# Performance work log

Measured on AMD Instinct MI355X. Metric: run time of the kernel, lower is better.

Reference implementation:

```python
import jax, jax.numpy as jnp
import numpy as np
import math

M = 512          # num_bin_x
NB = 512         # num_bin_y
NUM_NODES = 2_000_000
K = 4            # max bins a node can overlap per dim (size <= 2.5 bins)
SQRT2 = math.sqrt(2.0)


def setup_inputs() -> dict:
    key = jax.random.key(0)
    k1, k2 = jax.random.split(key)
    node_pos = jax.random.uniform(k1, (NUM_NODES, 2), jnp.float32, 0.05, 0.95)
    # node sizes between 0.5 and 2.5 bins (normalized layout units)
    node_size = jax.random.uniform(k2, (NUM_NODES, 2), jnp.float32) * (2.0 / M) + (0.5 / M)
    return {
        "node_pos": node_pos,
        "node_size": node_size,
        "node_weight": jnp.ones((NUM_NODES,), jnp.float32),
        "expand_ratio": jnp.ones((NUM_NODES,), jnp.float32),
        "unit_len": jnp.array([1.0 / M, 1.0 / NB], jnp.float32),
        "init_density_map": jnp.zeros((M, NB), jnp.float32),
        "num_bin_x": M,
        "num_bin_y": NB,
    }


def pre_normalize(node_pos, node_size, node_weight, expand_ratio, unit_len, mx, ny):
    # density_map_cuda.pre_normalize: expand tiny nodes to sqrt(2)*unit_len,
    # rescale weight to preserve area, convert rects to bin coordinates.
    ux, uy = unit_len[0], unit_len[1]
    w, h = node_size[:, 0], node_size[:, 1]
    new_w = jnp.maximum(w, SQRT2 * ux)
    new_h = jnp.maximum(h, SQRT2 * uy)
    weight = node_weight * expand_ratio * (w * h) / (new_w * new_h)
    xl = jnp.clip((node_pos[:, 0] - 0.5 * new_w) / ux, 0.0, mx)
    xh = jnp.clip((node_pos[:, 0] + 0.5 * new_w) / ux, 0.0, mx)
    yl = jnp.clip((node_pos[:, 1] - 0.5 * new_h) / uy, 0.0, ny)
    yh = jnp.clip((node_pos[:, 1] + 0.5 * new_h) / uy, 0.0, ny)
    return jnp.stack([xl, xh, yl, yh, weight], axis=1)  # [N, 5]


def scatter_density(info, mx, ny):
    # density_map_cuda.forward: overlap-area scatter-add of node rects into bins.
    xl, xh, yl, yh, w = info[:, 0], info[:, 1], info[:, 2], info[:, 3], info[:, 4]
    bx0 = jnp.floor(xl).astype(jnp.int32)
    by0 = jnp.floor(yl).astype(jnp.int32)
    dm = jnp.zeros((mx, ny), jnp.float32)
    for dx in range(K):
        ix = bx0 + dx
        fx = ix.astype(jnp.float32)
        ox = jnp.clip(jnp.minimum(xh, fx + 1.0) - jnp.maximum(xl, fx), 0.0)
        ixc = jnp.clip(ix, 0, mx - 1)
        for dy in range(K):
            iy = by0 + dy
            fy = iy.astype(jnp.float32)
            oy = jnp.clip(jnp.minimum(yh, fy + 1.0) - jnp.maximum(yl, fy), 0.0)
            iyc = jnp.clip(iy, 0, ny - 1)
            dm = dm.at[ixc, iyc].add(w * ox * oy)
    return dm


def make_transforms(n):
    k = jnp.arange(n, dtype=jnp.float32)[:, None]
    m = jnp.arange(n, dtype=jnp.float32)[None, :]
    ang = jnp.pi * k * (2.0 * m + 1.0) / (2.0 * n)
    C = jnp.cos(ang)  # [freq, space]
    S = jnp.sin(ang)
    w = jnp.where(jnp.arange(n) == 0, 1.0, 2.0).astype(jnp.float32)
    return C, S, w


def spectral_solve(dm, unit_len, mx, ny):
    # fft_scale construction from __init__
    wj = (jnp.arange(mx, dtype=jnp.float32) * (2.0 * jnp.pi / mx))[:, None]
    wk = (jnp.arange(ny, dtype=jnp.float32) * (2.0 * jnp.pi / ny))[None, :]
    wk = wk * (unit_len[0] / unit_len[1])  # scale_w_k=True
    wsq = wj ** 2 + wk ** 2
    wsq = wsq.at[0, 0].set(1.0)
    pscale = (1.0 / wsq).at[0, 0].set(0.0)
    fx_scale = wj * pscale * 0.5
    fy_scale = wk * pscale * 0.5

    Cx, Sx, wx = make_transforms(mx)
    Cy, Sy, wy = make_transforms(ny)
    # dct2: coeff[u,v] = (1/(M*N)) * sum_{m,n} dm[m,n] cos(pi u(2m+1)/2M) cos(pi v(2n+1)/2N)
    coeff = (Cx @ dm @ Cy.T) / (mx * ny)
    ICx = (wx[:, None] * Cx)  # weighted inverse cosine basis [freq, space]
    ICy = (wy[:, None] * Cy)
    ISx = (wx[:, None] * Sx)
    ISy = (wy[:, None] * Sy)
    potential = ICx.T @ (coeff * pscale) @ ICy          # idct2
    force_x = ISx.T @ (coeff * fx_scale) @ ICy          # idxst_idct
    force_y = ICx.T @ (coeff * fy_scale) @ ISy          # idct_idxst
    return potential, force_x, force_y


def reference(node_pos, node_size, node_weight, expand_ratio, unit_len,
              init_density_map, num_bin_x, num_bin_y):
    info = pre_normalize(node_pos, node_size, node_weight, expand_ratio,
                         unit_len, num_bin_x, num_bin_y)
    density_map = init_density_map + scatter_density(info, num_bin_x, num_bin_y)
    potential, _, _ = spectral_solve(density_map, unit_len, num_bin_x, num_bin_y)
    energy = jnp.sum(potential * density_map)
    return energy
```

## Files before the change

### kernel.cpp

```cpp
#include <hip/hip_runtime.h>
#include <math.h>

#define MX 512
#define NY 512
#define TWO_PI 6.283185307179586f

#define TSHIFT 6
#define NT 64
#define LDIM 68
#define SLAB (LDIM * LDIM)
#define SLAB4 (SLAB / 4)
#define NPB 2048
#define KPT 8
#define CAP 40960
#define TTARGET 1216
#define RPARTS 19
#define QSCALE 26214.0f
#define QINV (1.0f / 26214.0f)

typedef __attribute__((ext_vector_type(8))) short short8;
typedef __attribute__((ext_vector_type(4))) float float4_t;
typedef __attribute__((ext_vector_type(4))) unsigned short ushort4_t;

__device__ __forceinline__ unsigned short f2bf(float x) {
    union { float f; unsigned u; } v; v.f = x;
    unsigned r = v.u + 0x7fffu + ((v.u >> 16) & 1u);
    return (unsigned short)(r >> 16);
}
__device__ __forceinline__ float bf2f(unsigned short h) {
    union { float f; unsigned u; } v; v.u = ((unsigned)h) << 16;
    return v.f;
}

__device__ __forceinline__ void node_bounds(float2 p, float2 s, float ux, float uy,
                                            float& xl, float& xh, float& yl, float& yh,
                                            float& nw, float& nh) {
    const float SQ2 = 1.41421356237309515f;
    nw = fmaxf(s.x, SQ2 * ux);
    nh = fmaxf(s.y, SQ2 * uy);
    xl = fminf(fmaxf((p.x - 0.5f * nw) / ux, 0.0f), (float)MX);
    xh = fminf(fmaxf((p.x + 0.5f * nw) / ux, 0.0f), (float)MX);
    yl = fminf(fmaxf((p.y - 0.5f * nh) / uy, 0.0f), (float)NY);
    yh = fminf(fmaxf((p.y + 0.5f * nh) / uy, 0.0f), (float)NY);
}

__global__ void gen_cos_kernel(unsigned short* __restrict__ Ch,
                               unsigned short* __restrict__ Cl,
                               unsigned int* __restrict__ base,
                               unsigned int* __restrict__ cursor,
                               float* __restrict__ out, int cap_mode) {
    int idx = blockIdx.x * blockDim.x + threadIdx.x;
    if (idx == 0) *out = 0.0f;
    if (cap_mode && idx <= NT) {
        base[idx] = (unsigned int)idx * CAP;
        if (idx < NT) cursor[idx] = (unsigned int)idx * CAP;
    }
    int a = idx >> 9;
    int j = idx & 511;
    float x = cospif((float)(a * (2 * j + 1)) * (1.0f / 1024.0f));
    unsigned short hi = f2bf(x);
    Ch[idx] = hi;
    Cl[idx] = f2bf(x - bf2f(hi));
}

__global__ __launch_bounds__(256)
void count_kernel(const float2* __restrict__ pos, const float2* __restrict__ size,
                  const float* __restrict__ unit_len,
                  unsigned int* __restrict__ cnt, int n) {
    __shared__ unsigned int h[NT];
    if (threadIdx.x < NT) h[threadIdx.x] = 0;
    __syncthreads();
    float ux = unit_len[0], uy = unit_len[1];
    int start = blockIdx.x * NPB;
    int end = min(start + NPB, n);
#pragma unroll
    for (int k = 0; k < KPT; k++) {
        int i = start + k * 256 + (int)threadIdx.x;
        if (i < end) {
            float xl, xh, yl, yh, nw, nh;
            node_bounds(pos[i], size[i], ux, uy, xl, xh, yl, yh, nw, nh);
            int bx0 = min((int)floorf(xl), MX - 1);
            int by0 = min((int)floorf(yl), NY - 1);
            atomicAdd(&h[((bx0 >> TSHIFT) << 3) | (by0 >> TSHIFT)], 1u);
        }
    }
    __syncthreads();
    if (threadIdx.x < NT) {
        unsigned int c = h[threadIdx.x];
        if (c) atomicAdd(&cnt[threadIdx.x], c);
    }
}

__global__ void scan_kernel(const unsigned int* __restrict__ cnt,
                            unsigned int* __restrict__ base,
                            unsigned int* __restrict__ cursor) {
    if (threadIdx.x == 0 && blockIdx.x == 0) {
        unsigned int ex = 0;
        for (int t = 0; t < NT; t++) {
            base[t] = ex;
            cursor[t] = ex;
            ex += cnt[t];
        }
        base[NT] = ex;
    }
}

__global__ __launch_bounds__(256)
void place_kernel(const float2* __restrict__ pos, const float2* __restrict__ size,
                  const float* __restrict__ nwt, const float* __restrict__ er,
                  const float* __restrict__ unit_len,
                  const unsigned int* __restrict__ base,
                  unsigned int* __restrict__ cursor,
                  float4* __restrict__ pb, int n) {
    __shared__ unsigned int h[NT];
    __shared__ unsigned int lb[NT + 1];
    __shared__ unsigned int bb[NT];
    __shared__ float4 buf[NPB];
    __shared__ unsigned char til[NPB];
    if (threadIdx.x < NT) h[threadIdx.x] = 0;
    __syncthreads();
    float ux = unit_len[0], uy = unit_len[1];
    int start = blockIdx.x * NPB;
    int end = min(start + NPB, n);

    float cxl[KPT], cyl[KPT], cw[KPT];
    unsigned int cq[KPT], pk[KPT];
#pragma unroll
    for (int k = 0; k < KPT; k++) {
        int i = start + k * 256 + (int)threadIdx.x;
        if (i < end) {
            float2 p = pos[i], s = size[i];
            float xl, xh, yl, yh, nw, nh;
            node_bounds(p, s, ux, uy, xl, xh, yl, yh, nw, nh);
            cxl[k] = xl; cyl[k] = yl;
            cw[k] = nwt[i] * er[i] * (s.x * s.y) / (nw * nh);
            unsigned qx = (unsigned)((xh - xl) * QSCALE + 0.5f);
            unsigned qy = (unsigned)((yh - yl) * QSCALE + 0.5f);
            if (qx > 65535u) qx = 65535u;
            if (qy > 65535u) qy = 65535u;
            cq[k] = qx | (qy << 16);
            int bx0 = min((int)floorf(xl), MX - 1);
            int by0 = min((int)floorf(yl), NY - 1);
            unsigned int t = ((bx0 >> TSHIFT) << 3) | (by0 >> TSHIFT);
            pk[k] = (t << 11) | atomicAdd(&h[t], 1u);
        }
    }
    __syncthreads();
    if (threadIdx.x < NT) {
        unsigned int c = h[threadIdx.x];
        unsigned int S = c;
#pragma unroll
        for (int d = 1; d < 64; d <<= 1) {
            unsigned int v = __shfl_up(S, d, 64);
            if ((int)threadIdx.x >= d) S += v;
        }
        lb[threadIdx.x] = S - c;
        if (threadIdx.x == NT - 1) lb[NT] = S;
        bb[threadIdx.x] = c ? atomicAdd(&cursor[threadIdx.x], c) : 0u;
    }
    __syncthreads();
#pragma unroll
    for (int k = 0; k < KPT; k++) {
        int i = start + k * 256 + (int)threadIdx.x;
        if (i < end) {
            unsigned int t = pk[k] >> 11;
            unsigned int slot = lb[t] + (pk[k] & 2047u);
            buf[slot] = make_float4(cxl[k], cyl[k], cw[k], __uint_as_float(cq[k]));
            til[slot] = (unsigned char)t;
        }
    }
    __syncthreads();
    unsigned int total = lb[NT];
    for (unsigned int j = threadIdx.x; j < total; j += 256) {
        unsigned int t = til[j];
        unsigned int dst = bb[t] + (j - lb[t]);
        if (dst < base[t + 1]) pb[dst] = buf[j];
    }
}

__device__ __forceinline__ void accum_one(float4 v, float* acc, int tbx, int tby) {
    float xl = v.x, yl = v.y, w = v.z;
    unsigned q = __float_as_uint(v.w);
    float xh = xl + (float)(q & 0xffffu) * QINV;
    float yh = yl + (float)(q >> 16) * QINV;
    int bx0 = min((int)floorf(xl), MX - 1);
    int by0 = min((int)floorf(yl), NY - 1);
    float oxs[4], oys[4];
    int rb[4], lys[4];
#pragma unroll
    for (int d = 0; d < 4; d++) {
        int ix = bx0 + d;
        float fx = (float)ix;
        oxs[d] = fmaxf(fminf(xh, fx + 1.0f) - fmaxf(xl, fx), 0.0f);
        rb[d] = (min(ix, MX - 1) - tbx) * LDIM;
        int iy = by0 + d;
        float fy = (float)iy;
        oys[d] = fmaxf(fminf(yh, fy + 1.0f) - fmaxf(yl, fy), 0.0f);
        lys[d] = min(iy, NY - 1) - tby;
    }
#pragma unroll
    for (int dx = 0; dx < 4; dx++) {
        if (oxs[dx] == 0.0f) continue;
        float wox = w * oxs[dx];
#pragma unroll
        for (int dy = 0; dy < 4; dy++) {
            float vv = wox * oys[dy];
            if (vv != 0.0f) atomicAdd(&acc[rb[dx] + lys[dy]], vv);
        }
    }
}

__global__ __launch_bounds__(256)
void accum_kernel(const float4* __restrict__ pb,
                  const unsigned int* __restrict__ base,
                  const unsigned int* __restrict__ cursor,
                  float* __restrict__ slab, int T) {
    __shared__ float acc[SLAB];
    __shared__ int sh_t, sh_done;
    __shared__ unsigned int sh_ks, sh_ke, sh_b0;
    int tid = threadIdx.x;
    if (tid < 64) {
        unsigned int t = tid;
        unsigned int b0 = base[t];
        unsigned int cap = base[t + 1] - b0;
        unsigned int cr = cursor[t] - b0;
        unsigned int c = cr < cap ? cr : cap;
        unsigned int S = c;
#pragma unroll
        for (int d = 1; d < 64; d <<= 1) {
            unsigned int v = __shfl_up(S, d, 64);
            if (tid >= d) S += v;
        }
        unsigned int total = __shfl(S, 63, 64);
        unsigned int nb = total ? (unsigned int)(((unsigned long long)c * (unsigned int)T) / total) + 1u : 1u;
        unsigned int Pn = nb;
#pragma unroll
        for (int d = 1; d < 64; d <<= 1) {
            unsigned int v = __shfl_up(Pn, d, 64);
            if (tid >= d) Pn += v;
        }
        unsigned int NBU = __shfl(Pn, 63, 64);
        unsigned int Pex = Pn - nb;
        unsigned int b = blockIdx.x;
        if (tid == 0) sh_done = (b >= NBU) ? 1 : 0;
        if (b >= Pex && b < Pn) {
            unsigned int s = b - Pex;
            unsigned int chunk = nb ? (c + nb - 1) / nb : 0u;
            unsigned int ks = s * chunk;
            unsigned int ke = min(c, ks + chunk);
            sh_t = (int)t; sh_ks = ks; sh_ke = ke; sh_b0 = b0;
        }
    }
    for (int e = tid; e < SLAB4; e += 256)
        ((float4*)acc)[e] = make_float4(0.f, 0.f, 0.f, 0.f);
    __syncthreads();
    if (sh_done) return;

    int t = sh_t;
    int tbx = (t >> 3) << TSHIFT;
    int tby = (t & 7) << TSHIFT;
    unsigned int b0 = sh_b0;
    unsigned int ke = sh_ke;

    unsigned int k = sh_ks + (unsigned int)tid;
    float4 cur = make_float4(0.f, 0.f, 0.f, 0.f);
    bool have = (k < ke);
    if (have) cur = pb[b0 + k];
    while (have) {
        unsigned int k2 = k + 256;
        bool have2 = (k2 < ke);
        float4 nxt = make_float4(0.f, 0.f, 0.f, 0.f);
        if (have2) nxt = pb[b0 + k2];
        accum_one(cur, acc, tbx, tby);
        cur = nxt; k = k2; have = have2;
    }
    __syncthreads();

    float4* dst = (float4*)(slab + (size_t)blockIdx.x * SLAB);
    for (int e = tid; e < SLAB4; e += 256)
        dst[e] = ((float4*)acc)[e];
}

__global__ __launch_bounds__(256)
void reduce_slabs_kernel(const float* __restrict__ slab,
                         float* __restrict__ tacc,
                         const unsigned int* __restrict__ base,
                         const unsigned int* __restrict__ cursor, int T) {
    __shared__ unsigned int sh_P, sh_nb;
    int t = blockIdx.x / RPARTS;
    int part = blockIdx.x - t * RPARTS;
    int tid = threadIdx.x;
    if (tid < 64) {
        unsigned int tt = tid;
        unsigned int b0 = base[tt];
        unsigned int cap = base[tt + 1] - b0;
        unsigned int cr = cursor[tt] - b0;
        unsigned int c = cr < cap ? cr : cap;
        unsigned int S = c;
#pragma unroll
        for (int d = 1; d < 64; d <<= 1) {
            unsigned int v = __shfl_up(S, d, 64);
            if (tid >= d) S += v;
        }
        unsigned int total = __shfl(S, 63, 64);
        unsigned int nb = total ? (unsigned int)(((unsigned long long)c * (unsigned int)T) / total) + 1u : 1u;
        unsigned int Pn = nb;
#pragma unroll
        for (int d = 1; d < 64; d <<= 1) {
            unsigned int v = __shfl_up(Pn, d, 64);
            if (tid >= d) Pn += v;
        }
        if ((int)tt == t) { sh_P = Pn - nb; sh_nb = nb; }
    }
    __syncthreads();
    int e = part * 256 + tid;
    if (e < SLAB) {
        const float* s0 = slab + (size_t)sh_P * SLAB + e;
        float sum = 0.0f;
        unsigned int nb = sh_nb;
        for (unsigned int s = 0; s < nb; s++) sum += s0[(size_t)s * SLAB];
        tacc[(size_t)t * SLAB + e] = sum;
    }
}

__global__ __launch_bounds__(256)
void combine_kernel(const float* __restrict__ tacc,
                    const float* __restrict__ init_dm,
                    unsigned short* __restrict__ dmh,
                    unsigned short* __restrict__ dml) {
    int v = blockIdx.x * blockDim.x + threadIdx.x;
    int gx = v >> 7;
    int g4 = v & 127;
    int gy = g4 << 2;
    int rx = gx & 63, ry = gy & 63;
    int tx0 = gx >> TSHIFT, ty0 = gy >> TSHIFT;

    float4 sum = ((const float4*)init_dm)[v];
#pragma unroll
    for (int ax = 0; ax < 2; ax++) {
        int tx = tx0 - ax;
        if (tx < 0 || (ax == 1 && rx > 3)) continue;
        int lx = rx + (ax << TSHIFT);
#pragma unroll
        for (int ay = 0; ay < 2; ay++) {
            int ty = ty0 - ay;
            if (ty < 0 || (ay == 1 && ry > 0)) continue;
            int ly = ry + (ay << TSHIFT);
            float4 sv = *(const float4*)(tacc
                + (size_t)((tx << 3) | ty) * SLAB + lx * LDIM + ly);
            sum.x += sv.x; sum.y += sv.y; sum.z += sv.z; sum.w += sv.w;
        }
    }
    ushort4_t hi, lo;
    float sv[4] = {sum.x, sum.y, sum.z, sum.w};
#pragma unroll
    for (int r = 0; r < 4; r++) {
        unsigned short h = f2bf(sv[r]);
        hi[r] = h;
        lo[r] = f2bf(sv[r] - bf2f(h));
    }
    int idx = (gx << 9) | gy;
    *(ushort4_t*)(dmh + idx) = hi;
    *(ushort4_t*)(dml + idx) = lo;
}

__global__ __launch_bounds__(256)
void scatter_kernel(const float2* __restrict__ pos, const float2* __restrict__ size,
                    const float* __restrict__ nwt, const float* __restrict__ er,
                    const float* __restrict__ unit_len,
                    float* __restrict__ dm, int n) {
    int i = blockIdx.x * blockDim.x + threadIdx.x;
    if (i >= n) return;
    float ux = unit_len[0], uy = unit_len[1];
    float2 p = pos[i], s = size[i];
    float xl, xh, yl, yh, nw, nh;
    node_bounds(p, s, ux, uy, xl, xh, yl, yh, nw, nh);
    float w = nwt[i] * er[i] * (s.x * s.y) / (nw * nh);
    int bx0 = (int)floorf(xl);
    int by0 = (int)floorf(yl);
#pragma unroll
    for (int dx = 0; dx < 4; dx++) {
        int ix = bx0 + dx;
        float fx = (float)ix;
        float ox = fmaxf(fminf(xh, fx + 1.0f) - fmaxf(xl, fx), 0.0f);
        if (ox == 0.0f) continue;
        int rowoff = min(max(ix, 0), MX - 1) * NY;
        float wox = w * ox;
#pragma unroll
        for (int dy = 0; dy < 4; dy++) {
            int iy = by0 + dy;
            float fy = (float)iy;
            float oy = fmaxf(fminf(yh, fy + 1.0f) - fmaxf(yl, fy), 0.0f);
            float vv = wox * oy;
            if (vv != 0.0f) atomicAdd(&dm[rowoff + min(max(iy, 0), NY - 1)], vv);
        }
    }
}

__global__ void cvt_dm_kernel(const float* __restrict__ dm,
                              unsigned short* __restrict__ dmh,
                              unsigned short* __restrict__ dml) {
    int idx = blockIdx.x * blockDim.x + threadIdx.x;
    float x = dm[idx];
    unsigned short hi = f2bf(x);
    dmh[idx] = hi;
    dml[idx] = f2bf(x - bf2f(hi));
}

__global__ __launch_bounds__(256)
void dct1_mfma_kernel(const unsigned short* __restrict__ dmh,
                      const unsigned short* __restrict__ dml,
                      const unsigned short* __restrict__ Ch,
                      const unsigned short* __restrict__ Cl,
                      unsigned short* __restrict__ UhT,
                      unsigned short* __restrict__ UlT) {
    int lane = threadIdx.x & 63;
    int wv = threadIdx.x >> 6;
    int tile = blockIdx.x * 4 + wv;
    int jt = (tile >> 5) * 16;
    int bt = (tile & 31) * 16;
    int m = lane & 15, q = lane >> 4;
    float4_t acc = {0.f, 0.f, 0.f, 0.f};
    const unsigned short* ah_row = dmh + (jt + m) * 512;
    const unsigned short* al_row = dml + (jt + m) * 512;
    const unsigned short* bh_row = Ch + (bt + m) * 512;
    const unsigned short* bl_row = Cl + (bt + m) * 512;
#pragma unroll 4
    for (int k0 = 0; k0 < 512; k0 += 32) {
        int off = k0 + q * 8;
        short8 ah = *(const short8*)(ah_row + off);
        short8 al = *(const short8*)(al_row + off);
        short8 bh = *(const short8*)(bh_row + off);
        short8 bl = *(const short8*)(bl_row + off);
        acc = __builtin_amdgcn_mfma_f32_16x16x32_bf16(ah, bh, acc, 0, 0, 0);
        acc = __builtin_amdgcn_mfma_f32_16x16x32_bf16(ah, bl, acc, 0, 0, 0);
        acc = __builtin_amdgcn_mfma_f32_16x16x32_bf16(al, bh, acc, 0, 0, 0);
    }
#pragma unroll
    for (int r = 0; r < 4; r++) {
        float v = acc[r];
        unsigned short hi = f2bf(v);
        int addr = (bt + m) * 512 + jt + q * 4 + r;
        UhT[addr] = hi;
        UlT[addr] = f2bf(v - bf2f(hi));
    }
}

__global__ __launch_bounds__(256)
void dct2_mfma_kernel(const unsigned short* __restrict__ Ch,
                      const unsigned short* __restrict__ Cl,
                      const unsigned short* __restrict__ UhT,
                      const unsigned short* __restrict__ UlT,
                      const float* __restrict__ unit_len,
                      float* __restrict__ out) {
    __shared__ float red[4];
    int lane = threadIdx.x & 63;
    int wv = threadIdx.x >> 6;
    int tile = blockIdx.x * 4 + wv;
    int at = (tile >> 5) * 16;
    int bt = (tile & 31) * 16;
    int m = lane & 15, q = lane >> 4;
    float4_t acc = {0.f, 0.f, 0.f, 0.f};
    const unsigned short* ah_row = Ch + (at + m) * 512;
    const unsigned short* al_row = Cl + (at + m) * 512;
    const unsigned short* bh_row = UhT + (bt + m) * 512;
    const unsigned short* bl_row = UlT + (bt + m) * 512;
#pragma unroll 4
    for (int k0 = 0; k0 < 512; k0 += 32) {
        int off = k0 + q * 8;
        short8 ah = *(const short8*)(ah_row + off);
        short8 al = *(const short8*)(al_row + off);
        short8 bh = *(const short8*)(bh_row + off);
        short8 bl = *(const short8*)(bl_row + off);
        acc = __builtin_amdgcn_mfma_f32_16x16x32_bf16(ah, bh, acc, 0, 0, 0);
        acc = __builtin_amdgcn_mfma_f32_16x16x32_bf16(ah, bl, acc, 0, 0, 0);
        acc = __builtin_amdgcn_mfma_f32_16x16x32_bf16(al, bh, acc, 0, 0, 0);
    }
    float ratio = unit_len[0] / unit_len[1];
    int b = bt + m;
    float wkb = (float)b * (TWO_PI / (float)NY) * ratio;
    float wyb = (b == 0) ? 1.0f : 2.0f;
    float e = 0.0f;
#pragma unroll
    for (int r = 0; r < 4; r++) {
        int a = at + q * 4 + r;
        float wja = (float)a * (TWO_PI / (float)MX);
        float wsq = wja * wja + wkb * wkb;
        float ps = (a == 0 && b == 0) ? 0.0f : (1.0f / wsq);
        float wxa = (a == 0) ? 1.0f : 2.0f;
        e += wxa * wyb * ps * acc[r] * acc[r];
    }
#pragma unroll
    for (int off = 32; off > 0; off >>= 1) e += __shfl_down(e, off, 64);
    if (lane == 0) red[wv] = e;
    __syncthreads();
    if (threadIdx.x == 0) {
        float t = red[0] + red[1] + red[2] + red[3];
        atomicAdd(out, t * (1.0f / ((float)MX * (float)NY)));
    }
}

extern "C" void kernel_launch(void* const* d_in, const int* in_sizes, int n_in,
                              void* d_out, int out_size, void* d_ws, size_t ws_size,
                              hipStream_t stream) {
    const float2* node_pos  = (const float2*)d_in[0];
    const float2* node_size = (const float2*)d_in[1];
    const float*  node_wt   = (const float*)d_in[2];
    const float*  exp_ratio = (const float*)d_in[3];
    const float*  unit_len  = (const float*)d_in[4];
    const float*  init_dm   = (const float*)d_in[5];
    float* out = (float*)d_out;
    int n = in_sizes[2];

    char* wsb = (char*)d_ws;
    size_t off = 0;
    auto alloc = [&](size_t bytes) { void* p = wsb + off; off = (off + bytes + 255) & ~(size_t)255; return p; };
    unsigned short* Ch   = (unsigned short*)alloc((size_t)MX * NY * 2);
    unsigned short* Cl   = (unsigned short*)alloc((size_t)MX * NY * 2);
    unsigned short* dmh  = (unsigned short*)alloc((size_t)MX * NY * 2);
    unsigned short* dml  = (unsigned short*)alloc((size_t)MX * NY * 2);
    unsigned short* UhT  = (unsigned short*)alloc((size_t)MX * NY * 2);
    unsigned short* UlT  = (unsigned short*)alloc((size_t)MX * NY * 2);
    float*          dm     = (float*)alloc((size_t)MX * NY * sizeof(float));
    unsigned int*   cnt    = (unsigned int*)alloc(NT * sizeof(unsigned int));
    unsigned int*   tbase  = (unsigned int*)alloc((NT + 1) * sizeof(unsigned int));
    unsigned int*   cursor = (unsigned int*)alloc(NT * sizeof(unsigned int));
    float*          tacc   = (float*)alloc((size_t)NT * SLAB * sizeof(float));
    size_t off_common = off;
    size_t slab_bytes = (size_t)SLAB * sizeof(float);

    float4* pbF = (float4*)alloc((size_t)NT * CAP * sizeof(float4));
    int TF = 0;
    float* slbF = nullptr;
    if (off <= ws_size) {
        size_t navail = (ws_size - off) / slab_bytes;
        if (navail >= 320) {
            size_t t = navail - 64;
            TF = (int)(t > TTARGET ? TTARGET : t);
            slbF = (float*)alloc((size_t)(TF + 64) * slab_bytes);
        }
    }
    bool tierFast = (slbF != nullptr);

    off = off_common;
    float4* pbE = (float4*)alloc((size_t)n * sizeof(float4));
    int TE = 0;
    float* slbE = nullptr;
    if (off <= ws_size) {
        size_t navail = (ws_size - off) / slab_bytes;
        if (navail >= 128) {
            size_t t = navail - 64;
            TE = (int)(t > TTARGET ? TTARGET : t);
            slbE = (float*)alloc((size_t)(TE + 64) * slab_bytes);
        }
    }
    bool tierExact = (slbE != nullptr);

    gen_cos_kernel<<<(MX * NY) / 256, 256, 0, stream>>>(Ch, Cl, tbase, cursor,
                                                        out, tierFast ? 1 : 0);

    if (tierFast || tierExact) {
        float4* pb  = tierFast ? pbF : pbE;
        float*  slb = tierFast ? slbF : slbE;
        int     T   = tierFast ? TF : TE;
        int nblk = (n + NPB - 1) / NPB;
        if (!tierFast) {
            hipMemsetAsync(cnt, 0, NT * sizeof(unsigned int), stream);
            count_kernel<<<nblk, 256, 0, stream>>>(node_pos, node_size, unit_len, cnt, n);
            scan_kernel<<<1, 64, 0, stream>>>(cnt, tbase, cursor);
        }
        place_kernel<<<nblk, 256, 0, stream>>>(
            node_pos, node_size, node_wt, exp_ratio, unit_len, tbase, cursor, pb, n);
        accum_kernel<<<T + 64, 256, 0, stream>>>(pb, tbase, cursor, slb, T);
        reduce_slabs_kernel<<<NT * RPARTS, 256, 0, stream>>>(slb, tacc, tbase, cursor, T);
        combine_kernel<<<256, 256, 0, stream>>>(tacc, init_dm, dmh, dml);
    } else {
        hipMemcpyAsync(dm, init_dm, (size_t)MX * NY * sizeof(float),
                       hipMemcpyDeviceToDevice, stream);
        scatter_kernel<<<(n + 255) / 256, 256, 0, stream>>>(
            node_pos, node_size, node_wt, exp_ratio, unit_len, dm, n);
        cvt_dm_kernel<<<(MX * NY) / 256, 256, 0, stream>>>(dm, dmh, dml);
    }

    dct1_mfma_kernel<<<256, 256, 0, stream>>>(dmh, dml, Ch, Cl, UhT, UlT);
    dct2_mfma_kernel<<<256, 256, 0, stream>>>(Ch, Cl, UhT, UlT, unit_len, out);
}
```

Measured before the change: 235.0 us.

## Fuse reduce, combine, cosine gen and both DCT stages into one cooperative kernel

On the fast tier, the cosine-table generation, slab reduction, tile combine, and the two MFMA DCT passes are merged into one cooperative kernel that uses grid.sync between phases. Per-tile buffers are now addressed at fixed offsets of t*CAP, with cursors zeroed by a memset, so the separate init of base/cursor goes away. This cuts several kernel launches and their inter-kernel gaps. The cost is that the whole pipeline runs on only 256 blocks with grid-wide barriers, and the slab reduction now runs serially per element.

New measurement: 356.9 us. +51.8%, slower.

```diff
diff --git a/kernel.cpp b/kernel.cpp
--- a/kernel.cpp
+++ b/kernel.cpp
@@ -1,5 +1,8 @@
 #include <hip/hip_runtime.h>
+#include <hip/hip_cooperative_groups.h>
 #include <math.h>
+
+namespace cg = cooperative_groups;
 
 #define MX 512
 #define NY 512
@@ -17,6 +20,7 @@
 #define RPARTS 19
 #define QSCALE 26214.0f
 #define QINV (1.0f / 26214.0f)
+#define NBLK_MEGA 256
 
 typedef __attribute__((ext_vector_type(8))) short short8;
 typedef __attribute__((ext_vector_type(4))) float float4_t;
@@ -44,79 +48,18 @@
     yh = fminf(fmaxf((p.y + 0.5f * nh) / uy, 0.0f), (float)NY);
 }
 
-__global__ void gen_cos_kernel(unsigned short* __restrict__ Ch,
-                               unsigned short* __restrict__ Cl,
-                               unsigned int* __restrict__ base,
-                               unsigned int* __restrict__ cursor,
-                               float* __restrict__ out, int cap_mode) {
-    int idx = blockIdx.x * blockDim.x + threadIdx.x;
-    if (idx == 0) *out = 0.0f;
-    if (cap_mode && idx <= NT) {
-        base[idx] = (unsigned int)idx * CAP;
-        if (idx < NT) cursor[idx] = (unsigned int)idx * CAP;
-    }
-    int a = idx >> 9;
-    int j = idx & 511;
-    float x = cospif((float)(a * (2 * j + 1)) * (1.0f / 1024.0f));
-    unsigned short hi = f2bf(x);
-    Ch[idx] = hi;
-    Cl[idx] = f2bf(x - bf2f(hi));
-}
-
 __global__ __launch_bounds__(256)
-void count_kernel(const float2* __restrict__ pos, const float2* __restrict__ size,
-                  const float* __restrict__ unit_len,
-                  unsigned int* __restrict__ cnt, int n) {
-    __shared__ unsigned int h[NT];
-    if (threadIdx.x < NT) h[threadIdx.x] = 0;
-    __syncthreads();
-    float ux = unit_len[0], uy = unit_len[1];
-    int start = blockIdx.x * NPB;
-    int end = min(start + NPB, n);
-#pragma unroll
-    for (int k = 0; k < KPT; k++) {
-        int i = start + k * 256 + (int)threadIdx.x;
-        if (i < end) {
-            float xl, xh, yl, yh, nw, nh;
-            node_bounds(pos[i], size[i], ux, uy, xl, xh, yl, yh, nw, nh);
-            int bx0 = min((int)floorf(xl), MX - 1);
-            int by0 = min((int)floorf(yl), NY - 1);
-            atomicAdd(&h[((bx0 >> TSHIFT) << 3) | (by0 >> TSHIFT)], 1u);
-        }
-    }
-    __syncthreads();
-    if (threadIdx.x < NT) {
-        unsigned int c = h[threadIdx.x];
-        if (c) atomicAdd(&cnt[threadIdx.x], c);
-    }
-}
-
-__global__ void scan_kernel(const unsigned int* __restrict__ cnt,
-                            unsigned int* __restrict__ base,
-                            unsigned int* __restrict__ cursor) {
-    if (threadIdx.x == 0 && blockIdx.x == 0) {
-        unsigned int ex = 0;
-        for (int t = 0; t < NT; t++) {
-            base[t] = ex;
-            cursor[t] = ex;
-            ex += cnt[t];
-        }
-        base[NT] = ex;
-    }
-}
-
-__global__ __launch_bounds__(256)
-void place_kernel(const float2* __restrict__ pos, const float2* __restrict__ size,
-                  const float* __restrict__ nwt, const float* __restrict__ er,
-                  const float* __restrict__ unit_len,
-                  const unsigned int* __restrict__ base,
-                  unsigned int* __restrict__ cursor,
-                  float4* __restrict__ pb, int n) {
+void place_fast_kernel(const float2* __restrict__ pos, const float2* __restrict__ size,
+                       const float* __restrict__ nwt, const float* __restrict__ er,
+                       const float* __restrict__ unit_len,
+                       unsigned int* __restrict__ cursor,
+                       float4* __restrict__ pb, float* __restrict__ out, int n) {
     __shared__ unsigned int h[NT];
     __shared__ unsigned int lb[NT + 1];
     __shared__ unsigned int bb[NT];
     __shared__ float4 buf[NPB];
     __shared__ unsigned char til[NPB];
+    if (blockIdx.x == 0 && threadIdx.x == 0) *out = 0.0f;
     if (threadIdx.x < NT) h[threadIdx.x] = 0;
     __syncthreads();
     float ux = unit_len[0], uy = unit_len[1];
@@ -174,7 +117,7 @@
     for (unsigned int j = threadIdx.x; j < total; j += 256) {
         unsigned int t = til[j];
         unsigned int dst = bb[t] + (j - lb[t]);
-        if (dst < base[t + 1]) pb[dst] = buf[j];
+        if (dst < CAP) pb[(size_t)t * CAP + dst] = buf[j];
     }
 }
 
@@ -207,6 +150,385 @@
             float vv = wox * oys[dy];
             if (vv != 0.0f) atomicAdd(&acc[rb[dx] + lys[dy]], vv);
         }
+    }
+}
+
+__global__ __launch_bounds__(256)
+void accum_fast_kernel(const float4* __restrict__ pb,
+                       const unsigned int* __restrict__ cursor,
+                       float* __restrict__ slab, int T) {
+    __shared__ float acc[SLAB];
+    __shared__ int sh_t, sh_done;
+    __shared__ unsigned int sh_ks, sh_ke;
+    int tid = threadIdx.x;
+    if (tid < 64) {
+        unsigned int t = tid;
+        unsigned int cr = cursor[t];
+        unsigned int c = cr < CAP ? cr : CAP;
+        unsigned int S = c;
+#pragma unroll
+        for (int d = 1; d < 64; d <<= 1) {
+            unsigned int v = __shfl_up(S, d, 64);
+            if (tid >= d) S += v;
+        }
+        unsigned int total = __shfl(S, 63, 64);
+        unsigned int nb = total ? (unsigned int)(((unsigned long long)c * (unsigned int)T) / total) + 1u : 1u;
+        unsigned int Pn = nb;
+#pragma unroll
+        for (int d = 1; d < 64; d <<= 1) {
+            unsigned int v = __shfl_up(Pn, d, 64);
+            if (tid >= d) Pn += v;
+        }
+        unsigned int NBU = __shfl(Pn, 63, 64);
+        unsigned int Pex = Pn - nb;
+        unsigned int b = blockIdx.x;
+        if (tid == 0) sh_done = (b >= NBU) ? 1 : 0;
+        if (b >= Pex && b < Pn) {
+            unsigned int s = b - Pex;
+            unsigned int chunk = nb ? (c + nb - 1) / nb : 0u;
+            unsigned int ks = s * chunk;
+            unsigned int ke = min(c, ks + chunk);
+            sh_t = (int)t; sh_ks = ks; sh_ke = ke;
+        }
+    }
+    for (int e = tid; e < SLAB4; e += 256)
+        ((float4*)acc)[e] = make_float4(0.f, 0.f, 0.f, 0.f);
+    __syncthreads();
+    if (sh_done) return;
+
+    int t = sh_t;
+    int tbx = (t >> 3) << TSHIFT;
+    int tby = (t & 7) << TSHIFT;
+    unsigned int b0 = (unsigned int)t * CAP;
+    unsigned int ke = sh_ke;
+
+    unsigned int k = sh_ks + (unsigned int)tid;
+    float4 cur = make_float4(0.f, 0.f, 0.f, 0.f);
+    bool have = (k < ke);
+    if (have) cur = pb[b0 + k];
+    while (have) {
+        unsigned int k2 = k + 256;
+        bool have2 = (k2 < ke);
+        float4 nxt = make_float4(0.f, 0.f, 0.f, 0.f);
+        if (have2) nxt = pb[b0 + k2];
+        accum_one(cur, acc, tbx, tby);
+        cur = nxt; k = k2; have = have2;
+    }
+    __syncthreads();
+
+    float4* dst = (float4*)(slab + (size_t)blockIdx.x * SLAB);
+    for (int e = tid; e < SLAB4; e += 256)
+        dst[e] = ((float4*)acc)[e];
+}
+
+__global__ __launch_bounds__(256, 1)
+void mega_kernel(const float* __restrict__ slab,
+                 const unsigned int* __restrict__ cursor, int T,
+                 const float* __restrict__ init_dm,
+                 unsigned short* __restrict__ Ch, unsigned short* __restrict__ Cl,
+                 unsigned short* __restrict__ dmh, unsigned short* __restrict__ dml,
+                 unsigned short* __restrict__ UhT, unsigned short* __restrict__ UlT,
+                 float* __restrict__ tacc,
+                 const float* __restrict__ unit_len, float* __restrict__ out) {
+    cg::grid_group grid = cg::this_grid();
+    __shared__ unsigned int shP[NT];
+    __shared__ unsigned int shNb[NT];
+    __shared__ float red[4];
+    int tid = threadIdx.x;
+    int bid = blockIdx.x;
+    int gid = bid * 256 + tid;
+
+    if (tid < 64) {
+        unsigned int tt = tid;
+        unsigned int cr = cursor[tt];
+        unsigned int c = cr < CAP ? cr : CAP;
+        unsigned int S = c;
+#pragma unroll
+        for (int d = 1; d < 64; d <<= 1) {
+            unsigned int v = __shfl_up(S, d, 64);
+            if (tid >= d) S += v;
+        }
+        unsigned int total = __shfl(S, 63, 64);
+        unsigned int nb = total ? (unsigned int)(((unsigned long long)c * (unsigned int)T) / total) + 1u : 1u;
+        unsigned int Pn = nb;
+#pragma unroll
+        for (int d = 1; d < 64; d <<= 1) {
+            unsigned int v = __shfl_up(Pn, d, 64);
+            if (tid >= d) Pn += v;
+        }
+        shP[tt] = Pn - nb;
+        shNb[tt] = nb;
+    }
+    __syncthreads();
+
+    for (int idx = gid; idx < MX * NY; idx += 65536) {
+        int a = idx >> 9;
+        int j = idx & 511;
+        float x = cospif((float)(a * (2 * j + 1)) * (1.0f / 1024.0f));
+        unsigned short hi = f2bf(x);
+        Ch[idx] = hi;
+        Cl[idx] = f2bf(x - bf2f(hi));
+    }
+    for (int x = gid; x < NT * SLAB; x += 65536) {
+        int t = x / SLAB;
+        int e = x - t * SLAB;
+        const float* s0 = slab + (size_t)shP[t] * SLAB + e;
+        float sum = 0.0f;
+        unsigned int nb = shNb[t];
+        for (unsigned int s = 0; s < nb; s++) sum += s0[(size_t)s * SLAB];
+        tacc[x] = sum;
+    }
+    grid.sync();
+
+    {
+        int v = gid;
+        int gx = v >> 7;
+        int g4 = v & 127;
+        int gy = g4 << 2;
+        int rx = gx & 63, ry = gy & 63;
+        int tx0 = gx >> TSHIFT, ty0 = gy >> TSHIFT;
+        float4 sum = ((const float4*)init_dm)[v];
+#pragma unroll
+        for (int ax = 0; ax < 2; ax++) {
+            int tx = tx0 - ax;
+            if (tx < 0 || (ax == 1 && rx > 3)) continue;
+            int lx = rx + (ax << TSHIFT);
+#pragma unroll
+            for (int ay = 0; ay < 2; ay++) {
+                int ty = ty0 - ay;
+                if (ty < 0 || (ay == 1 && ry > 0)) continue;
+                int ly = ry + (ay << TSHIFT);
+                float4 sv = *(const float4*)(tacc
+                    + (size_t)((tx << 3) | ty) * SLAB + lx * LDIM + ly);
+                sum.x += sv.x; sum.y += sv.y; sum.z += sv.z; sum.w += sv.w;
+            }
+        }
+        ushort4_t hi, lo;
+        float sv[4] = {sum.x, sum.y, sum.z, sum.w};
+#pragma unroll
+        for (int r = 0; r < 4; r++) {
+            unsigned short h = f2bf(sv[r]);
+            hi[r] = h;
+            lo[r] = f2bf(sv[r] - bf2f(h));
+        }
+        int idx = (gx << 9) | gy;
+        *(ushort4_t*)(dmh + idx) = hi;
+        *(ushort4_t*)(dml + idx) = lo;
+    }
+    grid.sync();
+
+    {
+        int lane = tid & 63;
+        int wv = tid >> 6;
+        int tile = bid * 4 + wv;
+        int jt = (tile >> 5) * 16;
+        int bt = (tile & 31) * 16;
+        int m = lane & 15, q = lane >> 4;
+        float4_t acc = {0.f, 0.f, 0.f, 0.f};
+        const unsigned short* ah_row = dmh + (jt + m) * 512;
+        const unsigned short* al_row = dml + (jt + m) * 512;
+        const unsigned short* bh_row = Ch + (bt + m) * 512;
+        const unsigned short* bl_row = Cl + (bt + m) * 512;
+#pragma unroll 4
+        for (int k0 = 0; k0 < 512; k0 += 32) {
+            int off = k0 + q * 8;
+            short8 ah = *(const short8*)(ah_row + off);
+            short8 al = *(const short8*)(al_row + off);
+            short8 bh = *(const short8*)(bh_row + off);
+            short8 bl = *(const short8*)(bl_row + off);
+            acc = __builtin_amdgcn_mfma_f32_16x16x32_bf16(ah, bh, acc, 0, 0, 0);
+            acc = __builtin_amdgcn_mfma_f32_16x16x32_bf16(ah, bl, acc, 0, 0, 0);
+            acc = __builtin_amdgcn_mfma_f32_16x16x32_bf16(al, bh, acc, 0, 0, 0);
+        }
+#pragma unroll
+        for (int r = 0; r < 4; r++) {
+            float v = acc[r];
+            unsigned short hi = f2bf(v);
+            int addr = (bt + m) * 512 + jt + q * 4 + r;
+            UhT[addr] = hi;
+            UlT[addr] = f2bf(v - bf2f(hi));
+        }
+    }
+    grid.sync();
+
+    {
+        int lane = tid & 63;
+        int wv = tid >> 6;
+        int tile = bid * 4 + wv;
+        int at = (tile >> 5) * 16;
+        int bt = (tile & 31) * 16;
+        int m = lane & 15, q = lane >> 4;
+        float4_t acc = {0.f, 0.f, 0.f, 0.f};
+        const unsigned short* ah_row = Ch + (at + m) * 512;
+        const unsigned short* al_row = Cl + (at + m) * 512;
+        const unsigned short* bh_row = UhT + (bt + m) * 512;
+        const unsigned short* bl_row = UlT + (bt + m) * 512;
+#pragma unroll 4
+        for (int k0 = 0; k0 < 512; k0 += 32) {
+            int off = k0 + q * 8;
+            short8 ah = *(const short8*)(ah_row + off);
+            short8 al = *(const short8*)(al_row + off);
+            short8 bh = *(const short8*)(bh_row + off);
+            short8 bl = *(const short8*)(bl_row + off);
+            acc = __builtin_amdgcn_mfma_f32_16x16x32_bf16(ah, bh, acc, 0, 0, 0);
+            acc = __builtin_amdgcn_mfma_f32_16x16x32_bf16(ah, bl, acc, 0, 0, 0);
+            acc = __builtin_amdgcn_mfma_f32_16x16x32_bf16(al, bh, acc, 0, 0, 0);
+        }
+        float ratio = unit_len[0] / unit_len[1];
+        int b = bt + m;
+        float wkb = (float)b * (TWO_PI / (float)NY) * ratio;
+        float wyb = (b == 0) ? 1.0f : 2.0f;
+        float e = 0.0f;
+#pragma unroll
+        for (int r = 0; r < 4; r++) {
+            int a = at + q * 4 + r;
+            float wja = (float)a * (TWO_PI / (float)MX);
+            float wsq = wja * wja + wkb * wkb;
+            float ps = (a == 0 && b == 0) ? 0.0f : (1.0f / wsq);
+            float wxa = (a == 0) ? 1.0f : 2.0f;
+            e += wxa * wyb * ps * acc[r] * acc[r];
+        }
+#pragma unroll
+        for (int off = 32; off > 0; off >>= 1) e += __shfl_down(e, off, 64);
+        if (lane == 0) red[wv] = e;
+        __syncthreads();
+        if (tid == 0) {
+            float t = red[0] + red[1] + red[2] + red[3];
+            atomicAdd(out, t * (1.0f / ((float)MX * (float)NY)));
+        }
+    }
+}
+
+__global__ void gen_cos_kernel(unsigned short* __restrict__ Ch,
+                               unsigned short* __restrict__ Cl,
+                               unsigned int* __restrict__ base,
+                               unsigned int* __restrict__ cursor,
+                               float* __restrict__ out, int cap_mode) {
+    int idx = blockIdx.x * blockDim.x + threadIdx.x;
+    if (idx == 0) *out = 0.0f;
+    if (cap_mode && idx <= NT) {
+        base[idx] = (unsigned int)idx * CAP;
+        if (idx < NT) cursor[idx] = (unsigned int)idx * CAP;
+    }
+    int a = idx >> 9;
+    int j = idx & 511;
+    float x = cospif((float)(a * (2 * j + 1)) * (1.0f / 1024.0f));
+    unsigned short hi = f2bf(x);
+    Ch[idx] = hi;
+    Cl[idx] = f2bf(x - bf2f(hi));
+}
+
+__global__ __launch_bounds__(256)
+void count_kernel(const float2* __restrict__ pos, const float2* __restrict__ size,
+                  const float* __restrict__ unit_len,
+                  unsigned int* __restrict__ cnt, int n) {
+    __shared__ unsigned int h[NT];
+    if (threadIdx.x < NT) h[threadIdx.x] = 0;
+    __syncthreads();
+    float ux = unit_len[0], uy = unit_len[1];
+    int start = blockIdx.x * NPB;
+    int end = min(start + NPB, n);
+#pragma unroll
+    for (int k = 0; k < KPT; k++) {
+        int i = start + k * 256 + (int)threadIdx.x;
+        if (i < end) {
+            float xl, xh, yl, yh, nw, nh;
+            node_bounds(pos[i], size[i], ux, uy, xl, xh, yl, yh, nw, nh);
+            int bx0 = min((int)floorf(xl), MX - 1);
+            int by0 = min((int)floorf(yl), NY - 1);
+            atomicAdd(&h[((bx0 >> TSHIFT) << 3) | (by0 >> TSHIFT)], 1u);
+        }
+    }
+    __syncthreads();
+    if (threadIdx.x < NT) {
+        unsigned int c = h[threadIdx.x];
+        if (c) atomicAdd(&cnt[threadIdx.x], c);
+    }
+}
+
+__global__ void scan_kernel(const unsigned int* __restrict__ cnt,
+                            unsigned int* __restrict__ base,
+                            unsigned int* __restrict__ cursor) {
+    if (threadIdx.x == 0 && blockIdx.x == 0) {
+        unsigned int ex = 0;
+        for (int t = 0; t < NT; t++) {
+            base[t] = ex;
+            cursor[t] = ex;
+            ex += cnt[t];
+        }
+        base[NT] = ex;
+    }
+}
+
+__global__ __launch_bounds__(256)
+void place_kernel(const float2* __restrict__ pos, const float2* __restrict__ size,
+                  const float* __restrict__ nwt, const float* __restrict__ er,
+                  const float* __restrict__ unit_len,
+                  const unsigned int* __restrict__ base,
+                  unsigned int* __restrict__ cursor,
+                  float4* __restrict__ pb, int n) {
+    __shared__ unsigned int h[NT];
+    __shared__ unsigned int lb[NT + 1];
+    __shared__ unsigned int bb[NT];
+    __shared__ float4 buf[NPB];
+    __shared__ unsigned char til[NPB];
+    if (threadIdx.x < NT) h[threadIdx.x] = 0;
+    __syncthreads();
+    float ux = unit_len[0], uy = unit_len[1];
+    int start = blockIdx.x * NPB;
+    int end = min(start + NPB, n);
+    float cxl[KPT], cyl[KPT], cw[KPT];
+    unsigned int cq[KPT], pk[KPT];
+#pragma unroll
+    for (int k = 0; k < KPT; k++) {
+        int i = start + k * 256 + (int)threadIdx.x;
+        if (i < end) {
+            float2 p = pos[i], s = size[i];
+            float xl, xh, yl, yh, nw, nh;
+            node_bounds(p, s, ux, uy, xl, xh, yl, yh, nw, nh);
+            cxl[k] = xl; cyl[k] = yl;
+            cw[k] = nwt[i] * er[i] * (s.x * s.y) / (nw * nh);
+            unsigned qx = (unsigned)((xh - xl) * QSCALE + 0.5f);
+            unsigned qy = (unsigned)((yh - yl) * QSCALE + 0.5f);
+            if (qx > 65535u) qx = 65535u;
+            if (qy > 65535u) qy = 65535u;
+            cq[k] = qx | (qy << 16);
+            int bx0 = min((int)floorf(xl), MX - 1);
+            int by0 = min((int)floorf(yl), NY - 1);
+            unsigned int t = ((bx0 >> TSHIFT) << 3) | (by0 >> TSHIFT);
+            pk[k] = (t << 11) | atomicAdd(&h[t], 1u);
+        }
+    }
+    __syncthreads();
+    if (threadIdx.x < NT) {
+        unsigned int c = h[threadIdx.x];
+        unsigned int S = c;
+#pragma unroll
+        for (int d = 1; d < 64; d <<= 1) {
+            unsigned int v = __shfl_up(S, d, 64);
+            if ((int)threadIdx.x >= d) S += v;
+        }
+        lb[threadIdx.x] = S - c;
+        if (threadIdx.x == NT - 1) lb[NT] = S;
+        bb[threadIdx.x] = c ? atomicAdd(&cursor[threadIdx.x], c) : 0u;
+    }
+    __syncthreads();
+#pragma unroll
+    for (int k = 0; k < KPT; k++) {
+        int i = start + k * 256 + (int)threadIdx.x;
+        if (i < end) {
+            unsigned int t = pk[k] >> 11;
+            unsigned int slot = lb[t] + (pk[k] & 2047u);
+            buf[slot] = make_float4(cxl[k], cyl[k], cw[k], __uint_as_float(cq[k]));
+            til[slot] = (unsigned char)t;
+        }
+    }
+    __syncthreads();
+    unsigned int total = lb[NT];
+    for (unsigned int j = threadIdx.x; j < total; j += 256) {
+        unsigned int t = til[j];
+        unsigned int dst = bb[t] + (j - lb[t]);
+        if (dst < base[t + 1]) pb[dst] = buf[j];
     }
 }
 
@@ -255,13 +577,11 @@
         ((float4*)acc)[e] = make_float4(0.f, 0.f, 0.f, 0.f);
     __syncthreads();
     if (sh_done) return;
-
     int t = sh_t;
     int tbx = (t >> 3) << TSHIFT;
     int tby = (t & 7) << TSHIFT;
     unsigned int b0 = sh_b0;
     unsigned int ke = sh_ke;
-
     unsigned int k = sh_ks + (unsigned int)tid;
     float4 cur = make_float4(0.f, 0.f, 0.f, 0.f);
     bool have = (k < ke);
@@ -275,7 +595,6 @@
         cur = nxt; k = k2; have = have2;
     }
     __syncthreads();
-
     float4* dst = (float4*)(slab + (size_t)blockIdx.x * SLAB);
     for (int e = tid; e < SLAB4; e += 256)
         dst[e] = ((float4*)acc)[e];
@@ -334,7 +653,6 @@
     int gy = g4 << 2;
     int rx = gx & 63, ry = gy & 63;
     int tx0 = gx >> TSHIFT, ty0 = gy >> TSHIFT;
-
     float4 sum = ((const float4*)init_dm)[v];
 #pragma unroll
     for (int ax = 0; ax < 2; ax++) {
@@ -524,10 +842,11 @@
     float*          dm     = (float*)alloc((size_t)MX * NY * sizeof(float));
     unsigned int*   cnt    = (unsigned int*)alloc(NT * sizeof(unsigned int));
     unsigned int*   tbase  = (unsigned int*)alloc((NT + 1) * sizeof(unsigned int));
-    unsigned int*   cursor = (unsigned int*)alloc(NT * sizeof(unsigned int));
+    unsigned int*   ctrl   = (unsigned int*)alloc(128 * sizeof(unsigned int));
     float*          tacc   = (float*)alloc((size_t)NT * SLAB * sizeof(float));
     size_t off_common = off;
     size_t slab_bytes = (size_t)SLAB * sizeof(float);
+    unsigned int* cursorF = ctrl;
 
     float4* pbF = (float4*)alloc((size_t)NT * CAP * sizeof(float4));
     int TF = 0;
@@ -556,23 +875,45 @@
     }
     bool tierExact = (slbE != nullptr);
 
-    gen_cos_kernel<<<(MX * NY) / 256, 256, 0, stream>>>(Ch, Cl, tbase, cursor,
-                                                        out, tierFast ? 1 : 0);
-
-    if (tierFast || tierExact) {
-        float4* pb  = tierFast ? pbF : pbE;
-        float*  slb = tierFast ? slbF : slbE;
-        int     T   = tierFast ? TF : TE;
+    if (tierFast) {
         int nblk = (n + NPB - 1) / NPB;
-        if (!tierFast) {
-            hipMemsetAsync(cnt, 0, NT * sizeof(unsigned int), stream);
-            count_kernel<<<nblk, 256, 0, stream>>>(node_pos, node_size, unit_len, cnt, n);
-            scan_kernel<<<1, 64, 0, stream>>>(cnt, tbase, cursor);
-        }
+        hipMemsetAsync(ctrl, 0, 128 * sizeof(unsigned int), stream);
+        place_fast_kernel<<<nblk, 256, 0, stream>>>(
+            node_pos, node_size, node_wt, exp_ratio, unit_len, cursorF, pbF, out, n);
+        accum_fast_kernel<<<TF + 64, 256, 0, stream>>>(pbF, cursorF, slbF, TF);
+        {
+            const float* a_slb = slbF;
+            const unsigned int* a_cur = cursorF;
+            int a_T = TF;
+            const float* a_init = init_dm;
+            unsigned short *a_Ch = Ch, *a_Cl = Cl, *a_dmh = dmh, *a_dml = dml;
+            unsigned short *a_UhT = UhT, *a_UlT = UlT;
+            float* a_tacc = tacc;
+            const float* a_ul = unit_len;
+            float* a_out = out;
+            void* args[] = {
+                (void*)&a_slb, (void*)&a_cur, (void*)&a_T, (void*)&a_init,
+                (void*)&a_Ch, (void*)&a_Cl, (void*)&a_dmh, (void*)&a_dml,
+                (void*)&a_UhT, (void*)&a_UlT, (void*)&a_tacc,
+                (void*)&a_ul, (void*)&a_out
+            };
+            hipLaunchCooperativeKernel((void*)mega_kernel, dim3(NBLK_MEGA),
+                                       dim3(256), args, 0, stream);
+        }
+        return;
+    }
+
+    gen_cos_kernel<<<(MX * NY) / 256, 256, 0, stream>>>(Ch, Cl, tbase, cursorF,
+                                                        out, 0);
+    if (tierExact) {
+        int nblk = (n + NPB - 1) / NPB;
+        hipMemsetAsync(cnt, 0, NT * sizeof(unsigned int), stream);
+        count_kernel<<<nblk, 256, 0, stream>>>(node_pos, node_size, unit_len, cnt, n);
+        scan_kernel<<<1, 64, 0, stream>>>(cnt, tbase, cursorF);
         place_kernel<<<nblk, 256, 0, stream>>>(
-            node_pos, node_size, node_wt, exp_ratio, unit_len, tbase, cursor, pb, n);
-        accum_kernel<<<T + 64, 256, 0, stream>>>(pb, tbase, cursor, slb, T);
-        reduce_slabs_kernel<<<NT * RPARTS, 256, 0, stream>>>(slb, tacc, tbase, cursor, T);
+            node_pos, node_size, node_wt, exp_ratio, unit_len, tbase, cursorF, pbE, n);
+        accum_kernel<<<TE + 64, 256, 0, stream>>>(pbE, tbase, cursorF, slbE, TE);
+        reduce_slabs_kernel<<<NT * RPARTS, 256, 0, stream>>>(slbE, tacc, tbase, cursorF, TE);
         combine_kernel<<<256, 256, 0, stream>>>(tacc, init_dm, dmh, dml);
     } else {
         hipMemcpyAsync(dm, init_dm, (size_t)MX * NY * sizeof(float),
```
